# Kernel tuning notes

Measured on AMD Instinct MI355X. Metric: run time of the kernel, lower is better.

Reference implementation:

```python
import jax, jax.numpy as jnp
import numpy as np

B, T, C, H = 4, 1024, 768, 12
D = C // H  # head_dim = 64
NEG = -1e9  # finite stand-in for -inf mask logits (grad-safe)


def setup_inputs() -> dict:
    key = jax.random.key(0)
    ks = jax.random.split(key, 7)
    x = jax.random.normal(ks[0], (B, T, C), dtype=jnp.float32)
    # additive per-head bias [B,H,T,T]
    bias = jax.random.normal(ks[1], (B, H, T, T), dtype=jnp.float32)
    keep = jax.random.bernoulli(ks[2], 0.95, (B, 1, T, T))
    mask_logits = jnp.where(keep, 0.0, NEG).astype(jnp.float32)
    # parameters (torch nn.Linear: y = x @ W.T + b; store as [in,out] here)
    s_in = 1.0 / np.sqrt(C)
    W_qkv = jax.random.uniform(ks[3], (C, 3 * C), jnp.float32, -s_in, s_in)
    b_qkv = jnp.zeros((3 * C,), jnp.float32)
    W_proj = jax.random.uniform(ks[4], (C, C), jnp.float32, -s_in, s_in)
    b_proj = jnp.zeros((C,), jnp.float32)
    return {"x": x, "mask_logits": mask_logits, "bias": bias,
            "W_qkv": W_qkv, "b_qkv": b_qkv, "W_proj": W_proj, "b_proj": b_proj}


def reference(x, mask_logits, bias, W_qkv, b_qkv, W_proj, b_proj):
    scale = D ** (-0.5)
    qkv = x @ W_qkv + b_qkv                       # [B,T,3C]
    qkv = qkv.reshape(B, T, 3, H, D)
    q = jnp.transpose(qkv[:, :, 0], (0, 2, 1, 3))  # [B,H,T,D]
    k = jnp.transpose(qkv[:, :, 1], (0, 2, 1, 3))
    v = jnp.transpose(qkv[:, :, 2], (0, 2, 1, 3))
    logits = jnp.einsum('bhtd,bhsd->bhts', q, k) * scale  # [B,H,T,T]
    logits = logits + bias + mask_logits
    attn = jax.nn.softmax(logits, axis=-1)
    y = jnp.einsum('bhts,bhsd->bhtd', attn, v)    # [B,H,T,D]
    y = jnp.transpose(y, (0, 2, 1, 3)).reshape(B, T, C)
    y = y @ W_proj + b_proj
    return y, attn
```

## Files before the change

### kernel.cpp

```cpp
#include <hip/hip_runtime.h>
#include <stdint.h>

#define Bb 4
#define Tt 1024
#define Cc 768
#define Hh 12
#define Dd 64

typedef __attribute__((ext_vector_type(8))) short short8;
typedef __attribute__((ext_vector_type(4))) float f32x4;

__device__ inline unsigned short f2bf(float f) {
  union { float f; uint32_t u; } c; c.f = f;
  return (unsigned short)((c.u + 0x7FFFu + ((c.u >> 16) & 1u)) >> 16);
}

__global__ void k_convert(const float* __restrict__ in, unsigned short* __restrict__ out, int n4) {
  int i = blockIdx.x * blockDim.x + threadIdx.x;
  if (i >= n4) return;
  float4 v = ((const float4*)in)[i];
  ushort4 o;
  o.x = f2bf(v.x); o.y = f2bf(v.y); o.z = f2bf(v.z); o.w = f2bf(v.w);
  ((ushort4*)out)[i] = o;
}

__global__ void k_transpose(const float* __restrict__ W, unsigned short* __restrict__ WT,
                            int K, int N) {
  int i = blockIdx.x * blockDim.x + threadIdx.x;
  if (i >= N * K) return;
  int n = i / K, k = i - n * K;
  WT[i] = f2bf(W[k * N + n]);
}

#define BM 128
#define BN 128
#define BK 32
#define LDK 40

__global__ __launch_bounds__(256, 3) void k_gemm(
    const unsigned short* __restrict__ A, const unsigned short* __restrict__ B,
    const float* __restrict__ bias, int M, int N, int K, int mode,
    unsigned short* __restrict__ Qb, unsigned short* __restrict__ Kb,
    unsigned short* __restrict__ Vt, float* __restrict__ Y)
{
  __shared__ __align__(16) unsigned short Al[BM][LDK];
  __shared__ __align__(16) unsigned short Bl[BN][LDK];
  const int nb = N / BN;
  const int m0 = (blockIdx.x / nb) * BM;
  const int n0 = (blockIdx.x % nb) * BN;
  const int tid = threadIdx.x;
  const int lane = tid & 63;
  const int w = tid >> 6;
  const int wm = (w & 1) * 64;
  const int wn = (w >> 1) * 64;
  const int l16 = lane & 15, q = lane >> 4;

  f32x4 acc[4][4];
#pragma unroll
  for (int i = 0; i < 4; ++i)
#pragma unroll
    for (int j = 0; j < 4; ++j)
#pragma unroll
      for (int e = 0; e < 4; ++e) acc[i][j][e] = 0.f;

  const int rrow = tid >> 1;
  const int kch = (tid & 1) * 16;

  for (int k0 = 0; k0 < K; k0 += BK) {
    int4 va0 = *(const int4*)(A + (size_t)(m0 + rrow) * K + k0 + kch);
    int4 va1 = *(const int4*)(A + (size_t)(m0 + rrow) * K + k0 + kch + 8);
    int4 vb0 = *(const int4*)(B + (size_t)(n0 + rrow) * K + k0 + kch);
    int4 vb1 = *(const int4*)(B + (size_t)(n0 + rrow) * K + k0 + kch + 8);
    __syncthreads();
    *(int4*)(&Al[rrow][kch])     = va0;
    *(int4*)(&Al[rrow][kch + 8]) = va1;
    *(int4*)(&Bl[rrow][kch])     = vb0;
    *(int4*)(&Bl[rrow][kch + 8]) = vb1;
    __syncthreads();
    short8 af[4], bfr[4];
#pragma unroll
    for (int t = 0; t < 4; ++t) {
      af[t]  = *(const short8*)(&Al[wm + t * 16 + l16][q * 8]);
      bfr[t] = *(const short8*)(&Bl[wn + t * 16 + l16][q * 8]);
    }
#pragma unroll
    for (int i = 0; i < 4; ++i)
#pragma unroll
      for (int j = 0; j < 4; ++j)
        acc[i][j] = __builtin_amdgcn_mfma_f32_16x16x32_bf16(af[i], bfr[j], acc[i][j], 0, 0, 0);
  }

#pragma unroll
  for (int i = 0; i < 4; ++i)
#pragma unroll
    for (int j = 0; j < 4; ++j) {
      int mg = m0 + wm + i * 16 + q * 4;
      int ng = n0 + wn + j * 16 + l16;
      float bv = bias[ng];
#pragma unroll
      for (int r = 0; r < 4; ++r) {
        float v = acc[i][j][r] + bv;
        int mr = mg + r;
        if (mode == 0) {
          int which = ng / Cc;
          int nn = ng - which * Cc;
          int hh = nn >> 6, d = nn & 63;
          int bb = mr >> 10, t = mr & 1023;
          int bh = bb * Hh + hh;
          unsigned short o = f2bf(v);
          if (which == 0)      Qb[((size_t)bh * Tt + t) * Dd + d] = o;
          else if (which == 1) Kb[((size_t)bh * Tt + t) * Dd + d] = o;
          else                 Vt[((size_t)bh * Dd + d) * Tt + t] = o;
        } else {
          Y[(size_t)mr * N + ng] = v;
        }
      }
    }
}

__global__ __launch_bounds__(256, 2) void k_attn(
    const unsigned short* __restrict__ Qb, const unsigned short* __restrict__ Kb,
    const unsigned short* __restrict__ Vt,
    const float* __restrict__ bias, const float* __restrict__ mask,
    float* __restrict__ attn, unsigned short* __restrict__ Ob)
{
  __shared__ __align__(16) unsigned short Pl[4][32][136];
  __shared__ float red[4][32];
  __shared__ float rowmax[32];
  __shared__ float rowinv[32];

  const int bid = blockIdx.x;
  const int bh = bid >> 5;
  const int tile = bid & 31;
  const int b = bh / Hh;
  const int h = bh - b * Hh;
  const int row0 = tile * 32;
  const int tid = threadIdx.x, lane = tid & 63, w = tid >> 6;
  const int l16 = lane & 15, q = lane >> 4;
  const int colw = w * 256;

  const unsigned short* Qp = Qb + ((size_t)bh * Tt + row0) * Dd;
  const unsigned short* Kp = Kb + (size_t)bh * Tt * Dd;
  const unsigned short* Vp = Vt + (size_t)bh * Dd * Tt;
  const float* bp = bias + ((size_t)bh * Tt + row0) * Tt;
  const float* mp = mask + ((size_t)b * Tt + row0) * Tt;
  float* ap = attn + ((size_t)bh * Tt + row0) * Tt;

  short8 qf[2][2];
#pragma unroll
  for (int mt = 0; mt < 2; ++mt)
#pragma unroll
    for (int ks = 0; ks < 2; ++ks)
      qf[mt][ks] = *(const short8*)(Qp + (mt * 16 + l16) * Dd + ks * 32 + q * 8);

  f32x4 S[2][16];
#pragma unroll
  for (int mt = 0; mt < 2; ++mt)
#pragma unroll
    for (int nt = 0; nt < 16; ++nt)
#pragma unroll
      for (int e = 0; e < 4; ++e) S[mt][nt][e] = 0.f;

  __builtin_amdgcn_s_setprio(1);
#pragma unroll
  for (int nt = 0; nt < 16; ++nt) {
    int col = colw + nt * 16 + l16;
#pragma unroll
    for (int ks = 0; ks < 2; ++ks) {
      short8 kf = *(const short8*)(Kp + (size_t)col * Dd + ks * 32 + q * 8);
      S[0][nt] = __builtin_amdgcn_mfma_f32_16x16x32_bf16(kf, qf[0][ks], S[0][nt], 0, 0, 0);
      S[1][nt] = __builtin_amdgcn_mfma_f32_16x16x32_bf16(kf, qf[1][ks], S[1][nt], 0, 0, 0);
    }
  }
  __builtin_amdgcn_s_setprio(0);

#pragma unroll
  for (int mt = 0; mt < 2; ++mt) {
    const float* bR = bp + (size_t)(mt * 16 + l16) * Tt + colw + q * 4;
    const float* mR = mp + (size_t)(mt * 16 + l16) * Tt + colw + q * 4;
#pragma unroll
    for (int nt = 0; nt < 16; ++nt) {
      f32x4 bv = *(const f32x4*)(bR + nt * 16);
      f32x4 mv = *(const f32x4*)(mR + nt * 16);
      S[mt][nt] = S[mt][nt] * 0.125f + bv + mv;
    }
  }

#pragma unroll
  for (int mt = 0; mt < 2; ++mt) {
    float m = S[mt][0][0];
#pragma unroll
    for (int nt = 0; nt < 16; ++nt)
#pragma unroll
      for (int r = 0; r < 4; ++r) m = fmaxf(m, S[mt][nt][r]);
    m = fmaxf(m, __shfl_xor(m, 16, 64));
    m = fmaxf(m, __shfl_xor(m, 32, 64));
    if (q == 0) red[w][mt * 16 + l16] = m;
  }
  __syncthreads();
  if (tid < 32)
    rowmax[tid] = fmaxf(fmaxf(red[0][tid], red[1][tid]), fmaxf(red[2][tid], red[3][tid]));
  __syncthreads();

#pragma unroll
  for (int mt = 0; mt < 2; ++mt) {
    float m = rowmax[mt * 16 + l16];
    float s = 0.f;
#pragma unroll
    for (int nt = 0; nt < 16; ++nt)
#pragma unroll
      for (int r = 0; r < 4; ++r) {
        float p = __expf(S[mt][nt][r] - m);
        S[mt][nt][r] = p;
        s += p;
      }
    s += __shfl_xor(s, 16, 64);
    s += __shfl_xor(s, 32, 64);
    if (q == 0) red[w][mt * 16 + l16] = s;
  }
  __syncthreads();
  if (tid < 32)
    rowinv[tid] = 1.0f / (red[0][tid] + red[1][tid] + red[2][tid] + red[3][tid]);
  __syncthreads();

  f32x4 O[2][4];
#pragma unroll
  for (int mt = 0; mt < 2; ++mt)
#pragma unroll
    for (int dt = 0; dt < 4; ++dt)
#pragma unroll
      for (int e = 0; e < 4; ++e) O[mt][dt][e] = 0.f;

  for (int half = 0; half < 2; ++half) {
    __syncthreads();
#pragma unroll
    for (int mt = 0; mt < 2; ++mt) {
      float inv = rowinv[mt * 16 + l16];
      float* apR = ap + (size_t)(mt * 16 + l16) * Tt + colw + q * 4;
#pragma unroll
      for (int nn = 0; nn < 8; ++nn) {
        int nt = half * 8 + nn;
        f32x4 p = S[mt][nt] * inv;
        *(f32x4*)(apR + nt * 16) = p;
        ushort4 pb;
        pb.x = f2bf(p[0]); pb.y = f2bf(p[1]); pb.z = f2bf(p[2]); pb.w = f2bf(p[3]);
        *(ushort4*)(&Pl[w][mt * 16 + l16][nn * 16 + q * 4]) = pb;
      }
    }
    __syncthreads();
    __builtin_amdgcn_s_setprio(1);
#pragma unroll
    for (int kt = 0; kt < 4; ++kt) {
      short8 pf0 = *(const short8*)(&Pl[w][l16][kt * 32 + q * 8]);
      short8 pf1 = *(const short8*)(&Pl[w][16 + l16][kt * 32 + q * 8]);
#pragma unroll
      for (int dt = 0; dt < 4; ++dt) {
        short8 vf = *(const short8*)(Vp + (size_t)(dt * 16 + l16) * Tt
                                     + colw + half * 128 + kt * 32 + q * 8);
        O[0][dt] = __builtin_amdgcn_mfma_f32_16x16x32_bf16(pf0, vf, O[0][dt], 0, 0, 0);
        O[1][dt] = __builtin_amdgcn_mfma_f32_16x16x32_bf16(pf1, vf, O[1][dt], 0, 0, 0);
      }
    }
    __builtin_amdgcn_s_setprio(0);
  }

  __syncthreads();
  float* Op = (float*)&Pl[0][0][0] + w * 2048;
#pragma unroll
  for (int mt = 0; mt < 2; ++mt)
#pragma unroll
    for (int dt = 0; dt < 4; ++dt)
#pragma unroll
      for (int r = 0; r < 4; ++r) {
        int row = mt * 16 + q * 4 + r;
        int d = dt * 16 + l16;
        Op[row * 64 + d] = O[mt][dt][r];
      }
  __syncthreads();
  float* base = (float*)&Pl[0][0][0];
  for (int e = tid; e < 2048; e += 256) {
    float v = base[e] + base[2048 + e] + base[4096 + e] + base[6144 + e];
    int row = e >> 6, d = e & 63;
    Ob[((size_t)(b * Tt + row0 + row)) * Cc + h * Dd + d] = f2bf(v);
  }
}

extern "C" void kernel_launch(void* const* d_in, const int* in_sizes, int n_in,
                              void* d_out, int out_size, void* d_ws, size_t ws_size,
                              hipStream_t stream) {
  const float* x     = (const float*)d_in[0];
  const float* maskl = (const float*)d_in[1];
  const float* bias  = (const float*)d_in[2];
  const float* Wqkv  = (const float*)d_in[3];
  const float* bqkv  = (const float*)d_in[4];
  const float* Wproj = (const float*)d_in[5];
  const float* bproj = (const float*)d_in[6];
  float* y    = (float*)d_out;
  float* attn = y + (size_t)Bb * Tt * Cc;

  char* ws = (char*)d_ws;
  unsigned short* xb     = (unsigned short*)(ws);
  unsigned short* WqkvT  = (unsigned short*)(ws + 6291456);
  unsigned short* WprojT = (unsigned short*)(ws + 9830400);
  unsigned short* Qb     = (unsigned short*)(ws + 11010048);
  unsigned short* Kb     = (unsigned short*)(ws + 17301504);
  unsigned short* Vt     = (unsigned short*)(ws + 23592960);
  unsigned short* Ob     = (unsigned short*)(ws + 29884416);

  k_convert<<<3072, 256, 0, stream>>>(x, xb, 786432);
  k_transpose<<<6912, 256, 0, stream>>>(Wqkv, WqkvT, 768, 2304);
  k_transpose<<<2304, 256, 0, stream>>>(Wproj, WprojT, 768, 768);
  k_gemm<<<576, 256, 0, stream>>>(xb, WqkvT, bqkv, 4096, 2304, 768, 0,
                                  Qb, Kb, Vt, nullptr);
  k_attn<<<1536, 256, 0, stream>>>(Qb, Kb, Vt, bias, maskl, attn, Ob);
  k_gemm<<<192, 256, 0, stream>>>(Ob, WprojT, bproj, 4096, 768, 768, 1,
                                  nullptr, nullptr, nullptr, y);
}
```

Baseline: 536.3 us.

## Tile weight transposes, add separate V transpose, halve attention row tile

Weight transposes now go through a shared-memory 32x32 tile so both the reads and the writes are coalesced. The QKV GEMM writes V in row-major layout into a scratch buffer, and a new kernel transposes it into Vt, replacing the strided scattered stores. The attention kernel now handles 16 query rows per block instead of 32, which doubles the grid and raises launch bounds to 3 blocks per SM for higher occupancy. In exchange, each K and V load is reused by half as many rows, so K/V reads double, and there is one extra kernel launch.

```diff
diff --git a/kernel.cpp b/kernel.cpp
--- a/kernel.cpp
+++ b/kernel.cpp
@@ -26,10 +26,36 @@
 
 __global__ void k_transpose(const float* __restrict__ W, unsigned short* __restrict__ WT,
                             int K, int N) {
-  int i = blockIdx.x * blockDim.x + threadIdx.x;
-  if (i >= N * K) return;
-  int n = i / K, k = i - n * K;
-  WT[i] = f2bf(W[k * N + n]);
+  __shared__ float tile[32][33];
+  const int nb = N >> 5;
+  const int bx = blockIdx.x % nb;
+  const int by = blockIdx.x / nb;
+  const int tx = threadIdx.x & 31, ty = threadIdx.x >> 5;
+#pragma unroll
+  for (int i = 0; i < 4; ++i)
+    tile[ty + i * 8][tx] = W[(size_t)(by * 32 + ty + i * 8) * N + bx * 32 + tx];
+  __syncthreads();
+#pragma unroll
+  for (int i = 0; i < 4; ++i)
+    WT[(size_t)(bx * 32 + ty + i * 8) * K + by * 32 + tx] = f2bf(tile[tx][ty + i * 8]);
+}
+
+__global__ void k_vtrans(const unsigned short* __restrict__ Vb, unsigned short* __restrict__ Vt) {
+  __shared__ unsigned short tile[32][34];
+  const int bid = blockIdx.x;
+  const int bh = bid >> 6;
+  const int ttile = (bid >> 1) & 31;
+  const int dtile = bid & 1;
+  const int tx = threadIdx.x & 31, ty = threadIdx.x >> 5;
+  const unsigned short* src = Vb + ((size_t)bh * Tt + ttile * 32) * Dd + dtile * 32;
+#pragma unroll
+  for (int i = 0; i < 4; ++i)
+    tile[ty + i * 8][tx] = src[(size_t)(ty + i * 8) * Dd + tx];
+  __syncthreads();
+  unsigned short* dst = Vt + ((size_t)bh * Dd + dtile * 32) * Tt + ttile * 32;
+#pragma unroll
+  for (int i = 0; i < 4; ++i)
+    dst[(size_t)(ty + i * 8) * Tt + tx] = tile[tx][ty + i * 8];
 }
 
 #define BM 128
@@ -41,7 +67,7 @@
     const unsigned short* __restrict__ A, const unsigned short* __restrict__ B,
     const float* __restrict__ bias, int M, int N, int K, int mode,
     unsigned short* __restrict__ Qb, unsigned short* __restrict__ Kb,
-    unsigned short* __restrict__ Vt, float* __restrict__ Y)
+    unsigned short* __restrict__ Vb, float* __restrict__ Y)
 {
   __shared__ __align__(16) unsigned short Al[BM][LDK];
   __shared__ __align__(16) unsigned short Bl[BN][LDK];
@@ -108,9 +134,8 @@
           int bb = mr >> 10, t = mr & 1023;
           int bh = bb * Hh + hh;
           unsigned short o = f2bf(v);
-          if (which == 0)      Qb[((size_t)bh * Tt + t) * Dd + d] = o;
-          else if (which == 1) Kb[((size_t)bh * Tt + t) * Dd + d] = o;
-          else                 Vt[((size_t)bh * Dd + d) * Tt + t] = o;
+          unsigned short* dst = (which == 0) ? Qb : (which == 1) ? Kb : Vb;
+          dst[((size_t)bh * Tt + t) * Dd + d] = o;
         } else {
           Y[(size_t)mr * N + ng] = v;
         }
@@ -118,23 +143,23 @@
     }
 }
 
-__global__ __launch_bounds__(256, 2) void k_attn(
+__global__ __launch_bounds__(256, 3) void k_attn(
     const unsigned short* __restrict__ Qb, const unsigned short* __restrict__ Kb,
     const unsigned short* __restrict__ Vt,
     const float* __restrict__ bias, const float* __restrict__ mask,
     float* __restrict__ attn, unsigned short* __restrict__ Ob)
 {
-  __shared__ __align__(16) unsigned short Pl[4][32][136];
-  __shared__ float red[4][32];
-  __shared__ float rowmax[32];
-  __shared__ float rowinv[32];
+  __shared__ __align__(16) unsigned short Pl[4][16][136];
+  __shared__ float red[4][16];
+  __shared__ float rowmax[16];
+  __shared__ float rowinv[16];
 
   const int bid = blockIdx.x;
-  const int bh = bid >> 5;
-  const int tile = bid & 31;
+  const int bh = bid >> 6;
+  const int tile = bid & 63;
   const int b = bh / Hh;
   const int h = bh - b * Hh;
-  const int row0 = tile * 32;
+  const int row0 = tile * 16;
   const int tid = threadIdx.x, lane = tid & 63, w = tid >> 6;
   const int l16 = lane & 15, q = lane >> 4;
   const int colw = w * 256;
@@ -146,20 +171,16 @@
   const float* mp = mask + ((size_t)b * Tt + row0) * Tt;
   float* ap = attn + ((size_t)bh * Tt + row0) * Tt;
 
-  short8 qf[2][2];
-#pragma unroll
-  for (int mt = 0; mt < 2; ++mt)
-#pragma unroll
-    for (int ks = 0; ks < 2; ++ks)
-      qf[mt][ks] = *(const short8*)(Qp + (mt * 16 + l16) * Dd + ks * 32 + q * 8);
-
-  f32x4 S[2][16];
-#pragma unroll
-  for (int mt = 0; mt < 2; ++mt)
-#pragma unroll
-    for (int nt = 0; nt < 16; ++nt)
-#pragma unroll
-      for (int e = 0; e < 4; ++e) S[mt][nt][e] = 0.f;
+  short8 qf[2];
+#pragma unroll
+  for (int ks = 0; ks < 2; ++ks)
+    qf[ks] = *(const short8*)(Qp + l16 * Dd + ks * 32 + q * 8);
+
+  f32x4 S[16];
+#pragma unroll
+  for (int nt = 0; nt < 16; ++nt)
+#pragma unroll
+    for (int e = 0; e < 4; ++e) S[nt][e] = 0.f;
 
   __builtin_amdgcn_s_setprio(1);
 #pragma unroll
@@ -168,118 +189,107 @@
 #pragma unroll
     for (int ks = 0; ks < 2; ++ks) {
       short8 kf = *(const short8*)(Kp + (size_t)col * Dd + ks * 32 + q * 8);
-      S[0][nt] = __builtin_amdgcn_mfma_f32_16x16x32_bf16(kf, qf[0][ks], S[0][nt], 0, 0, 0);
-      S[1][nt] = __builtin_amdgcn_mfma_f32_16x16x32_bf16(kf, qf[1][ks], S[1][nt], 0, 0, 0);
+      S[nt] = __builtin_amdgcn_mfma_f32_16x16x32_bf16(kf, qf[ks], S[nt], 0, 0, 0);
     }
   }
   __builtin_amdgcn_s_setprio(0);
 
-#pragma unroll
-  for (int mt = 0; mt < 2; ++mt) {
-    const float* bR = bp + (size_t)(mt * 16 + l16) * Tt + colw + q * 4;
-    const float* mR = mp + (size_t)(mt * 16 + l16) * Tt + colw + q * 4;
+  {
+    const float* bR = bp + (size_t)l16 * Tt + colw + q * 4;
+    const float* mR = mp + (size_t)l16 * Tt + colw + q * 4;
 #pragma unroll
     for (int nt = 0; nt < 16; ++nt) {
       f32x4 bv = *(const f32x4*)(bR + nt * 16);
       f32x4 mv = *(const f32x4*)(mR + nt * 16);
-      S[mt][nt] = S[mt][nt] * 0.125f + bv + mv;
-    }
-  }
-
-#pragma unroll
-  for (int mt = 0; mt < 2; ++mt) {
-    float m = S[mt][0][0];
+      S[nt] = S[nt] * 0.125f + bv + mv;
+    }
+  }
+
+  {
+    float m = S[0][0];
 #pragma unroll
     for (int nt = 0; nt < 16; ++nt)
 #pragma unroll
-      for (int r = 0; r < 4; ++r) m = fmaxf(m, S[mt][nt][r]);
+      for (int r = 0; r < 4; ++r) m = fmaxf(m, S[nt][r]);
     m = fmaxf(m, __shfl_xor(m, 16, 64));
     m = fmaxf(m, __shfl_xor(m, 32, 64));
-    if (q == 0) red[w][mt * 16 + l16] = m;
-  }
-  __syncthreads();
-  if (tid < 32)
+    if (q == 0) red[w][l16] = m;
+  }
+  __syncthreads();
+  if (tid < 16)
     rowmax[tid] = fmaxf(fmaxf(red[0][tid], red[1][tid]), fmaxf(red[2][tid], red[3][tid]));
   __syncthreads();
 
-#pragma unroll
-  for (int mt = 0; mt < 2; ++mt) {
-    float m = rowmax[mt * 16 + l16];
+  {
+    float m = rowmax[l16];
     float s = 0.f;
 #pragma unroll
     for (int nt = 0; nt < 16; ++nt)
 #pragma unroll
       for (int r = 0; r < 4; ++r) {
-        float p = __expf(S[mt][nt][r] - m);
-        S[mt][nt][r] = p;
+        float p = __expf(S[nt][r] - m);
+        S[nt][r] = p;
         s += p;
       }
     s += __shfl_xor(s, 16, 64);
     s += __shfl_xor(s, 32, 64);
-    if (q == 0) red[w][mt * 16 + l16] = s;
-  }
-  __syncthreads();
-  if (tid < 32)
+    if (q == 0) red[w][l16] = s;
+  }
+  __syncthreads();
+  if (tid < 16)
     rowinv[tid] = 1.0f / (red[0][tid] + red[1][tid] + red[2][tid] + red[3][tid]);
   __syncthreads();
 
-  f32x4 O[2][4];
-#pragma unroll
-  for (int mt = 0; mt < 2; ++mt)
-#pragma unroll
-    for (int dt = 0; dt < 4; ++dt)
-#pragma unroll
-      for (int e = 0; e < 4; ++e) O[mt][dt][e] = 0.f;
-
+  f32x4 O[4];
+#pragma unroll
+  for (int dt = 0; dt < 4; ++dt)
+#pragma unroll
+    for (int e = 0; e < 4; ++e) O[dt][e] = 0.f;
+
+  const float inv = rowinv[l16];
   for (int half = 0; half < 2; ++half) {
     __syncthreads();
-#pragma unroll
-    for (int mt = 0; mt < 2; ++mt) {
-      float inv = rowinv[mt * 16 + l16];
-      float* apR = ap + (size_t)(mt * 16 + l16) * Tt + colw + q * 4;
+    {
+      float* apR = ap + (size_t)l16 * Tt + colw + q * 4;
 #pragma unroll
       for (int nn = 0; nn < 8; ++nn) {
         int nt = half * 8 + nn;
-        f32x4 p = S[mt][nt] * inv;
+        f32x4 p = S[nt] * inv;
         *(f32x4*)(apR + nt * 16) = p;
         ushort4 pb;
         pb.x = f2bf(p[0]); pb.y = f2bf(p[1]); pb.z = f2bf(p[2]); pb.w = f2bf(p[3]);
-        *(ushort4*)(&Pl[w][mt * 16 + l16][nn * 16 + q * 4]) = pb;
+        *(ushort4*)(&Pl[w][l16][nn * 16 + q * 4]) = pb;
       }
     }
     __syncthreads();
     __builtin_amdgcn_s_setprio(1);
 #pragma unroll
     for (int kt = 0; kt < 4; ++kt) {
-      short8 pf0 = *(const short8*)(&Pl[w][l16][kt * 32 + q * 8]);
-      short8 pf1 = *(const short8*)(&Pl[w][16 + l16][kt * 32 + q * 8]);
+      short8 pf = *(const short8*)(&Pl[w][l16][kt * 32 + q * 8]);
 #pragma unroll
       for (int dt = 0; dt < 4; ++dt) {
         short8 vf = *(const short8*)(Vp + (size_t)(dt * 16 + l16) * Tt
                                      + colw + half * 128 + kt * 32 + q * 8);
-        O[0][dt] = __builtin_amdgcn_mfma_f32_16x16x32_bf16(pf0, vf, O[0][dt], 0, 0, 0);
-        O[1][dt] = __builtin_amdgcn_mfma_f32_16x16x32_bf16(pf1, vf, O[1][dt], 0, 0, 0);
+        O[dt] = __builtin_amdgcn_mfma_f32_16x16x32_bf16(pf, vf, O[dt], 0, 0, 0);
       }
     }
     __builtin_amdgcn_s_setprio(0);
   }
 
   __syncthreads();
-  float* Op = (float*)&Pl[0][0][0] + w * 2048;
-#pragma unroll
-  for (int mt = 0; mt < 2; ++mt)
-#pragma unroll
-    for (int dt = 0; dt < 4; ++dt)
-#pragma unroll
-      for (int r = 0; r < 4; ++r) {
-        int row = mt * 16 + q * 4 + r;
-        int d = dt * 16 + l16;
-        Op[row * 64 + d] = O[mt][dt][r];
-      }
+  float* Op = (float*)&Pl[0][0][0] + w * 1024;
+#pragma unroll
+  for (int dt = 0; dt < 4; ++dt)
+#pragma unroll
+    for (int r = 0; r < 4; ++r) {
+      int row = q * 4 + r;
+      int d = dt * 16 + l16;
+      Op[row * 64 + d] = O[dt][r];
+    }
   __syncthreads();
   float* base = (float*)&Pl[0][0][0];
-  for (int e = tid; e < 2048; e += 256) {
-    float v = base[e] + base[2048 + e] + base[4096 + e] + base[6144 + e];
+  for (int e = tid; e < 1024; e += 256) {
+    float v = base[e] + base[1024 + e] + base[2048 + e] + base[3072 + e];
     int row = e >> 6, d = e & 63;
     Ob[((size_t)(b * Tt + row0 + row)) * Cc + h * Dd + d] = f2bf(v);
   }
@@ -306,13 +316,15 @@
   unsigned short* Kb     = (unsigned short*)(ws + 17301504);
   unsigned short* Vt     = (unsigned short*)(ws + 23592960);
   unsigned short* Ob     = (unsigned short*)(ws + 29884416);
+  unsigned short* Vb     = Ob;
 
   k_convert<<<3072, 256, 0, stream>>>(x, xb, 786432);
-  k_transpose<<<6912, 256, 0, stream>>>(Wqkv, WqkvT, 768, 2304);
-  k_transpose<<<2304, 256, 0, stream>>>(Wproj, WprojT, 768, 768);
+  k_transpose<<<1728, 256, 0, stream>>>(Wqkv, WqkvT, 768, 2304);
+  k_transpose<<<576, 256, 0, stream>>>(Wproj, WprojT, 768, 768);
   k_gemm<<<576, 256, 0, stream>>>(xb, WqkvT, bqkv, 4096, 2304, 768, 0,
-                                  Qb, Kb, Vt, nullptr);
-  k_attn<<<1536, 256, 0, stream>>>(Qb, Kb, Vt, bias, maskl, attn, Ob);
+                                  Qb, Kb, Vb, nullptr);
+  k_vtrans<<<3072, 256, 0, stream>>>(Vb, Vt);
+  k_attn<<<3072, 256, 0, stream>>>(Qb, Kb, Vt, bias, maskl, attn, Ob);
   k_gemm<<<192, 256, 0, stream>>>(Ob, WprojT, bproj, 4096, 768, 768, 1,
                                   nullptr, nullptr, nullptr, y);
 }
```

After: 538.7 us. No clear change (+0.4%).
